# Performance work log

Hardware: AMD Instinct MI355X
Metric: run time of the kernel (lower is better)

## Reference

```python
import jax, jax.numpy as jnp
import numpy as np

EPS = 1e-8  # torch.cosine_similarity eps
TEMPERATURE = 1.0


def setup_inputs() -> dict:
    key = jax.random.key(0)
    ks = jax.random.split(key, 12)
    B = 16384
    inp = {
        "user_ids": jax.random.randint(ks[0], (B, 8), 0, 100000),
        "item_ids": jax.random.randint(ks[1], (B, 4), 0, 50000),
        "sample_weight": jax.random.uniform(ks[2], (B,), jnp.float32, 0.01, 1.0),
        "user_table": jax.random.normal(ks[3], (100000, 64), jnp.float32) * 0.05,
        "item_table": jax.random.normal(ks[4], (50000, 64), jnp.float32) * 0.05,
        "uW1": jax.random.normal(ks[5], (512, 256), jnp.float32) * 0.04,
        "ub1": jnp.zeros((256,), jnp.float32),
        "uW2": jax.random.normal(ks[6], (256, 128), jnp.float32) * 0.06,
        "ub2": jnp.zeros((128,), jnp.float32),
        "iW1": jax.random.normal(ks[7], (256, 256), jnp.float32) * 0.06,
        "ib1": jnp.zeros((256,), jnp.float32),
        "iW2": jax.random.normal(ks[8], (256, 128), jnp.float32) * 0.06,
        "ib2": jnp.zeros((128,), jnp.float32),
        "n_neg": 3,
    }
    return inp


def _tower(ids, table, W1, b1, W2, b2):
    # embedding lookup [B, F, D] -> concat -> [B, F*D], then 2-layer relu MLP
    B = ids.shape[0]
    e = table[ids].reshape(B, -1)
    h = jax.nn.relu(e @ W1 + b1)
    return jax.nn.relu(h @ W2 + b2)


def reference(user_ids, item_ids, sample_weight, user_table, item_table,
              uW1, ub1, uW2, ub2, iW1, ib1, iW2, ib2, n_neg):
    u = _tower(user_ids, user_table, uW1, ub1, uW2, ub2)  # [B, 128]
    v = _tower(item_ids, item_table, iW1, ib1, iW2, ib2)  # [B, 128]
    # cosine similarity per row (torch eps clamp on norms)
    un = jnp.maximum(jnp.linalg.norm(u, axis=1), EPS)
    vn = jnp.maximum(jnp.linalg.norm(v, axis=1), EPS)
    y = jnp.sum(u * v, axis=1) / (un * vn)
    # sampling-bias correction
    y = y - jnp.log(sample_weight)
    # vectorized wrap-around in-batch negative gather:
    # scores[i] = [y[i], y[(i+1)%B], ..., y[(i+n_neg)%B]]
    B = y.shape[0]
    idx = (jnp.arange(B)[:, None] + jnp.arange(n_neg + 1)[None, :]) % B
    scores = y[idx] / TEMPERATURE  # [B, 1+n_neg]
    return scores
```

## Files before the change

kernel.cpp:

```cpp
#include <hip/hip_runtime.h>
#include <math.h>

#define CEPS 1e-8f

typedef __attribute__((ext_vector_type(8))) short bf16x8;
typedef __attribute__((ext_vector_type(4))) float f32x4;
typedef __attribute__((ext_vector_type(4))) unsigned int u32x4;
typedef __attribute__((ext_vector_type(2))) unsigned int u32x2;

__device__ __forceinline__ unsigned short f2bf(float f) {
    unsigned u = __builtin_bit_cast(unsigned, f);
    u += 0x7fffu + ((u >> 16) & 1u);
    return (unsigned short)(u >> 16);
}

__global__ __launch_bounds__(256)
void pack_all(const float* __restrict__ uW1, const float* __restrict__ uW2,
              const float* __restrict__ iW1, const float* __restrict__ iW2,
              unsigned short* __restrict__ o1, unsigned short* __restrict__ o2,
              unsigned short* __restrict__ o3, unsigned short* __restrict__ o4)
{
    int g = blockIdx.x * 256 + threadIdx.x;
    const float* src; unsigned short* dst; int N; int base;
    if (g < 16384)      { src = uW1; dst = o1; N = 256; base = 0;     }
    else if (g < 20480) { src = uW2; dst = o2; N = 128; base = 16384; }
    else if (g < 28672) { src = iW1; dst = o3; N = 256; base = 20480; }
    else                { src = iW2; dst = o4; N = 128; base = 28672; }
    int i = g - base;
    int kg = i / N, n = i - kg * N;
    unsigned short tmp[8];
    #pragma unroll
    for (int j = 0; j < 8; ++j)
        tmp[j] = f2bf(src[(kg * 8 + j) * N + n]);
    *reinterpret_cast<bf16x8*>(dst + ((size_t)i << 3)) =
        *reinterpret_cast<bf16x8*>(tmp);
}


template<int F>
__device__ __forceinline__ void stage_emb(const int* __restrict__ ids,
                                          const float* __restrict__ table,
                                          unsigned short* e_s, int row0, int tid)
{
    constexpr int FC = F * 8;
    constexpr int IT = (32 * FC) / 512;
    int idv[IT];
    #pragma unroll
    for (int it = 0; it < IT; ++it) {
        int c = tid + it * 512;
        int r = c / FC, f = (c % FC) >> 3;
        idv[it] = ids[(row0 + r) * F + f];
    }
    #pragma unroll
    for (int it = 0; it < IT; ++it) {
        int c = tid + it * 512;
        int r = c / FC, rem = c % FC;
        const float* src = table + (size_t)idv[it] * 64 + (rem & 7) * 8;
        float4 aa = *reinterpret_cast<const float4*>(src);
        float4 bb = *reinterpret_cast<const float4*>(src + 4);
        u32x4 pk;
        pk.x = f2bf(aa.x) | ((unsigned)f2bf(aa.y) << 16);
        pk.y = f2bf(aa.z) | ((unsigned)f2bf(aa.w) << 16);
        pk.z = f2bf(bb.x) | ((unsigned)f2bf(bb.y) << 16);
        pk.w = f2bf(bb.z) | ((unsigned)f2bf(bb.w) << 16);
        int byte = r * (F * 128) + rem * 16;
        byte ^= (r & 7) << 4;
        *reinterpret_cast<u32x4*>(reinterpret_cast<char*>(e_s) + byte) = pk;
    }
}

template<int KB>
__device__ __forceinline__ bf16x8 loadA(const unsigned short* s, int ks, int ni,
                                        int l15, int l4)
{
    int row = ni * 16 + l15;
    int byte = row * (KB * 2) + ks * 64 + l4 * 16;
    byte ^= (row & 7) << 4;
    return *reinterpret_cast<const bf16x8*>(
               reinterpret_cast<const char*>(s) + byte);
}

template<int K1>
__device__ __forceinline__ void gemm1(
    const unsigned short* e_s, unsigned short* h_s,
    const unsigned short* __restrict__ W1p, const float* __restrict__ b1,
    int l15, int l4, int wl, const bf16x8 (&w01)[2][4])
{
    constexpr int NKS = K1 / 32;
    f32x4 acc[4][2];
    #pragma unroll
    for (int mi = 0; mi < 4; ++mi)
        #pragma unroll
        for (int ni = 0; ni < 2; ++ni) acc[mi][ni] = (f32x4){0.f, 0.f, 0.f, 0.f};

    const unsigned short* Wbase = W1p + ((l4 * 256 + wl * 64 + l15) << 3);
    bf16x8 wf[3][4], ef[2][2];
    #pragma unroll
    for (int mi = 0; mi < 4; ++mi) {
        wf[0][mi] = w01[0][mi];
        wf[1][mi] = w01[1][mi];
    }
    #pragma unroll
    for (int ni = 0; ni < 2; ++ni) ef[0][ni] = loadA<K1>(e_s, 0, ni, l15, l4);

    #pragma unroll
    for (int ks = 0; ks < NKS; ++ks) {
        if (ks + 2 < NKS) {
            #pragma unroll
            for (int mi = 0; mi < 4; ++mi)
                wf[(ks + 2) % 3][mi] = *reinterpret_cast<const bf16x8*>(
                    Wbase + (ks + 2) * 8192 + (mi << 7));
        }
        if (ks + 1 < NKS) {
            #pragma unroll
            for (int ni = 0; ni < 2; ++ni)
                ef[(ks + 1) & 1][ni] = loadA<K1>(e_s, ks + 1, ni, l15, l4);
        }
        __builtin_amdgcn_s_setprio(1);
        #pragma unroll
        for (int mi = 0; mi < 4; ++mi)
            #pragma unroll
            for (int ni = 0; ni < 2; ++ni)
                acc[mi][ni] = __builtin_amdgcn_mfma_f32_16x16x32_bf16(
                                  wf[ks % 3][mi], ef[ks & 1][ni], acc[mi][ni], 0, 0, 0);
        __builtin_amdgcn_s_setprio(0);
    }
    #pragma unroll
    for (int mi = 0; mi < 4; ++mi) {
        const float4 bb = *reinterpret_cast<const float4*>(
                              &b1[wl * 64 + mi * 16 + l4 * 4]);
        #pragma unroll
        for (int ni = 0; ni < 2; ++ni) {
            float v0 = acc[mi][ni][0] + bb.x; v0 = v0 > 0.f ? v0 : 0.f;
            float v1 = acc[mi][ni][1] + bb.y; v1 = v1 > 0.f ? v1 : 0.f;
            float v2 = acc[mi][ni][2] + bb.z; v2 = v2 > 0.f ? v2 : 0.f;
            float v3 = acc[mi][ni][3] + bb.w; v3 = v3 > 0.f ? v3 : 0.f;
            u32x2 d;
            d.x = f2bf(v0) | ((unsigned)f2bf(v1) << 16);
            d.y = f2bf(v2) | ((unsigned)f2bf(v3) << 16);
            int row = ni * 16 + l15;
            int w0c = wl * 64 + mi * 16 + l4 * 4;
            int byte = (row * 256 + w0c) * 2;
            byte ^= (row & 7) << 4;
            *reinterpret_cast<u32x2*>(reinterpret_cast<char*>(h_s) + byte) = d;
        }
    }
}

__device__ __forceinline__ void gemm2(
    const unsigned short* h_s, const unsigned short* __restrict__ W2p,
    f32x4 (&acc)[2][2], int l15, int l4, int wl, const bf16x8 (&w01)[2][2])
{
    #pragma unroll
    for (int mi = 0; mi < 2; ++mi)
        #pragma unroll
        for (int ni = 0; ni < 2; ++ni) acc[mi][ni] = (f32x4){0.f, 0.f, 0.f, 0.f};

    const unsigned short* Wbase = W2p + ((l4 * 128 + wl * 32 + l15) << 3);
    bf16x8 wf[3][2], hf[2][2];
    #pragma unroll
    for (int mi = 0; mi < 2; ++mi) {
        wf[0][mi] = w01[0][mi];
        wf[1][mi] = w01[1][mi];
    }
    #pragma unroll
    for (int ni = 0; ni < 2; ++ni) hf[0][ni] = loadA<256>(h_s, 0, ni, l15, l4);

    #pragma unroll
    for (int ks = 0; ks < 8; ++ks) {
        if (ks + 2 < 8) {
            #pragma unroll
            for (int mi = 0; mi < 2; ++mi)
                wf[(ks + 2) % 3][mi] = *reinterpret_cast<const bf16x8*>(
                    Wbase + (ks + 2) * 4096 + (mi << 7));
        }
        if (ks + 1 < 8) {
            #pragma unroll
            for (int ni = 0; ni < 2; ++ni)
                hf[(ks + 1) & 1][ni] = loadA<256>(h_s, ks + 1, ni, l15, l4);
        }
        __builtin_amdgcn_s_setprio(1);
        #pragma unroll
        for (int mi = 0; mi < 2; ++mi)
            #pragma unroll
            for (int ni = 0; ni < 2; ++ni)
                acc[mi][ni] = __builtin_amdgcn_mfma_f32_16x16x32_bf16(
                                  wf[ks % 3][mi], hf[ks & 1][ni], acc[mi][ni], 0, 0, 0);
        __builtin_amdgcn_s_setprio(0);
    }
}

__global__ __launch_bounds__(512, 4)
void fused_sbc(const int* __restrict__ user_ids,  const int* __restrict__ item_ids,
               const float* __restrict__ user_table, const float* __restrict__ item_table,
               const unsigned short* __restrict__ uW1p, const float* __restrict__ ub1,
               const unsigned short* __restrict__ uW2p, const float* __restrict__ ub2,
               const unsigned short* __restrict__ iW1p, const float* __restrict__ ib1,
               const unsigned short* __restrict__ iW2p, const float* __restrict__ ib2,
               const float* __restrict__ sw, float* __restrict__ out,
               int B, int nn1)
{
    __shared__ __align__(16) unsigned short smem[40960];
    unsigned short* e_u = smem;
    unsigned short* e_i = smem + 16384;
    unsigned short* h_u = smem + 24576;
    unsigned short* h_i = smem + 32768;
    float* V_lds = reinterpret_cast<float*>(smem);
    float* red   = reinterpret_cast<float*>(smem + 16384);

    const int tid  = threadIdx.x;
    const int lane = tid & 63;
    const int w    = tid >> 6;
    const int l15  = lane & 15, l4 = lane >> 4;
    const int role = w >> 2;
    const int wl   = w & 3;
    const int row0 = blockIdx.x * 32;

    const unsigned short* W1sel = role ? iW1p : uW1p;
    const unsigned short* W2sel = role ? iW2p : uW2p;

    bf16x8 w1pre[2][4];
    {
        const unsigned short* base = W1sel + ((l4 * 256 + wl * 64 + l15) << 3);
        #pragma unroll
        for (int s = 0; s < 2; ++s)
            #pragma unroll
            for (int mi = 0; mi < 4; ++mi)
                w1pre[s][mi] = *reinterpret_cast<const bf16x8*>(
                                   base + s * 8192 + (mi << 7));
    }
    stage_emb<8>(user_ids, user_table, e_u, row0, tid);
    stage_emb<4>(item_ids, item_table, e_i, row0, tid);
    __syncthreads();

    if (role == 0) gemm1<512>(e_u, h_u, uW1p, ub1, l15, l4, wl, w1pre);
    else           gemm1<256>(e_i, h_i, iW1p, ib1, l15, l4, wl, w1pre);

    bf16x8 w2pre[2][2];
    {
        const unsigned short* base = W2sel + ((l4 * 128 + wl * 32 + l15) << 3);
        #pragma unroll
        for (int s = 0; s < 2; ++s)
            #pragma unroll
            for (int mi = 0; mi < 2; ++mi)
                w2pre[s][mi] = *reinterpret_cast<const bf16x8*>(
                                   base + s * 4096 + (mi << 7));
    }
    __syncthreads();

    f32x4 acc2[2][2];
    if (role == 0) gemm2(h_u, uW2p, acc2, l15, l4, wl, w2pre);
    else           gemm2(h_i, iW2p, acc2, l15, l4, wl, w2pre);

    if (role == 1) {
        float pv[2] = {0.f, 0.f};
        #pragma unroll
        for (int mi = 0; mi < 2; ++mi) {
            const int colb = wl * 32 + mi * 16 + l4 * 4;
            const float4 bv = *reinterpret_cast<const float4*>(&ib2[colb]);
            #pragma unroll
            for (int ni = 0; ni < 2; ++ni) {
                int row = ni * 16 + l15;
                float v0 = acc2[mi][ni][0] + bv.x; v0 = v0 > 0.f ? v0 : 0.f;
                float v1 = acc2[mi][ni][1] + bv.y; v1 = v1 > 0.f ? v1 : 0.f;
                float v2 = acc2[mi][ni][2] + bv.z; v2 = v2 > 0.f ? v2 : 0.f;
                float v3 = acc2[mi][ni][3] + bv.w; v3 = v3 > 0.f ? v3 : 0.f;
                float4 vv = {v0, v1, v2, v3};
                *reinterpret_cast<float4*>(&V_lds[row * 132 + colb]) = vv;
                pv[ni] += v0 * v0 + v1 * v1 + v2 * v2 + v3 * v3;
            }
        }
        #pragma unroll
        for (int ni = 0; ni < 2; ++ni) {
            pv[ni] += __shfl_xor(pv[ni], 16);
            pv[ni] += __shfl_xor(pv[ni], 32);
        }
        if (l4 == 0) {
            #pragma unroll
            for (int ni = 0; ni < 2; ++ni)
                red[(wl * 32 + ni * 16 + l15) * 3 + 2] = pv[ni];
        }
    }
    __syncthreads();

    if (role == 0) {
        float pd[2] = {0.f, 0.f}, pu[2] = {0.f, 0.f};
        #pragma unroll
        for (int mi = 0; mi < 2; ++mi) {
            const int colb = wl * 32 + mi * 16 + l4 * 4;
            const float4 bu = *reinterpret_cast<const float4*>(&ub2[colb]);
            #pragma unroll
            for (int ni = 0; ni < 2; ++ni) {
                int row = ni * 16 + l15;
                float u0 = acc2[mi][ni][0] + bu.x; u0 = u0 > 0.f ? u0 : 0.f;
                float u1 = acc2[mi][ni][1] + bu.y; u1 = u1 > 0.f ? u1 : 0.f;
                float u2 = acc2[mi][ni][2] + bu.z; u2 = u2 > 0.f ? u2 : 0.f;
                float u3 = acc2[mi][ni][3] + bu.w; u3 = u3 > 0.f ? u3 : 0.f;
                const float4 vv = *reinterpret_cast<const float4*>(
                                      &V_lds[row * 132 + colb]);
                pd[ni] += u0 * vv.x + u1 * vv.y + u2 * vv.z + u3 * vv.w;
                pu[ni] += u0 * u0 + u1 * u1 + u2 * u2 + u3 * u3;
            }
        }
        #pragma unroll
        for (int ni = 0; ni < 2; ++ni) {
            pd[ni] += __shfl_xor(pd[ni], 16);
            pd[ni] += __shfl_xor(pd[ni], 32);
            pu[ni] += __shfl_xor(pu[ni], 16);
            pu[ni] += __shfl_xor(pu[ni], 32);
        }
        if (l4 == 0) {
            #pragma unroll
            for (int ni = 0; ni < 2; ++ni) {
                red[(wl * 32 + ni * 16 + l15) * 3 + 0] = pd[ni];
                red[(wl * 32 + ni * 16 + l15) * 3 + 1] = pu[ni];
            }
        }
    }
    __syncthreads();

    if (tid < 32) {
        int row = tid;
        float d = 0.f, su = 0.f, sv = 0.f;
        #pragma unroll
        for (int cg = 0; cg < 4; ++cg) {
            d  += red[(cg * 32 + row) * 3 + 0];
            su += red[(cg * 32 + row) * 3 + 1];
            sv += red[(cg * 32 + row) * 3 + 2];
        }
        float un = fmaxf(sqrtf(su), CEPS);
        float vn = fmaxf(sqrtf(sv), CEPS);
        int grow = row0 + row;
        float yv = d / (un * vn) - logf(sw[grow]);
        for (int j = 0; j < nn1; ++j) {
            int idx = grow - j;
            if (idx < 0) idx += B;
            out[idx * nn1 + j] = yv;
        }
    }
}

extern "C" void kernel_launch(void* const* d_in, const int* in_sizes, int n_in,
                              void* d_out, int out_size, void* d_ws, size_t ws_size,
                              hipStream_t stream)
{
    const int*   user_ids   = (const int*)  d_in[0];
    const int*   item_ids   = (const int*)  d_in[1];
    const float* sw         = (const float*)d_in[2];
    const float* user_table = (const float*)d_in[3];
    const float* item_table = (const float*)d_in[4];
    const float* uW1        = (const float*)d_in[5];
    const float* ub1        = (const float*)d_in[6];
    const float* uW2        = (const float*)d_in[7];
    const float* ub2        = (const float*)d_in[8];
    const float* iW1        = (const float*)d_in[9];
    const float* ib1        = (const float*)d_in[10];
    const float* iW2        = (const float*)d_in[11];
    const float* ib2        = (const float*)d_in[12];

    const int B   = in_sizes[2];
    const int nn1 = out_size / B;

    unsigned short* wp   = (unsigned short*)d_ws;
    unsigned short* uW1p = wp;
    unsigned short* uW2p = wp + 131072;
    unsigned short* iW1p = wp + 163840;
    unsigned short* iW2p = wp + 229376;
    float* out = (float*)d_out;

    pack_all<<<128, 256, 0, stream>>>(uW1, uW2, iW1, iW2,
                                      uW1p, uW2p, iW1p, iW2p);
    fused_sbc<<<B / 32, 512, 0, stream>>>(user_ids, item_ids,
                                          user_table, item_table,
                                          uW1p, ub1, uW2p, ub2,
                                          iW1p, ib1, iW2p, ib2,
                                          sw, out, B, nn1);
}
```

Baseline: 28.02 us.

## Feed first GEMM directly from embedding gathers, dropping the LDS staging

Removes the cooperative embedding staging into LDS and the barrier before the first GEMM. Each wave now gathers its own embedding rows from global memory straight into registers, converts them to bf16 with a cheaper rounding routine, and feeds them to the MFMAs with double-buffered prefetch. This cuts shared memory use (allowing more occupancy) and removes one sync, but every wave re-gathers the same embedding rows redundantly (four waves per role share rows), and the weight prefetch depth drops from two stages to one. The new bf16 rounding is round-half-up rather than round-to-nearest-even, which slightly changes numerics.

```diff
diff --git a/kernel.cpp b/kernel.cpp
--- a/kernel.cpp
+++ b/kernel.cpp
@@ -12,6 +12,21 @@
     unsigned u = __builtin_bit_cast(unsigned, f);
     u += 0x7fffu + ((u >> 16) & 1u);
     return (unsigned short)(u >> 16);
+}
+
+__device__ __forceinline__ unsigned pk2(float a, float b) {
+    unsigned ua = __builtin_bit_cast(unsigned, a) + 0x8000u;
+    unsigned ub = __builtin_bit_cast(unsigned, b) + 0x8000u;
+    return (ua >> 16) | (ub & 0xFFFF0000u);
+}
+
+__device__ __forceinline__ bf16x8 cvt8(const float4& lo, const float4& hi) {
+    u32x4 r;
+    r.x = pk2(lo.x, lo.y);
+    r.y = pk2(lo.z, lo.w);
+    r.z = pk2(hi.x, hi.y);
+    r.w = pk2(hi.z, hi.w);
+    return __builtin_bit_cast(bf16x8, r);
 }
 
 __global__ __launch_bounds__(256)
@@ -37,38 +52,6 @@
 }
 
 
-template<int F>
-__device__ __forceinline__ void stage_emb(const int* __restrict__ ids,
-                                          const float* __restrict__ table,
-                                          unsigned short* e_s, int row0, int tid)
-{
-    constexpr int FC = F * 8;
-    constexpr int IT = (32 * FC) / 512;
-    int idv[IT];
-    #pragma unroll
-    for (int it = 0; it < IT; ++it) {
-        int c = tid + it * 512;
-        int r = c / FC, f = (c % FC) >> 3;
-        idv[it] = ids[(row0 + r) * F + f];
-    }
-    #pragma unroll
-    for (int it = 0; it < IT; ++it) {
-        int c = tid + it * 512;
-        int r = c / FC, rem = c % FC;
-        const float* src = table + (size_t)idv[it] * 64 + (rem & 7) * 8;
-        float4 aa = *reinterpret_cast<const float4*>(src);
-        float4 bb = *reinterpret_cast<const float4*>(src + 4);
-        u32x4 pk;
-        pk.x = f2bf(aa.x) | ((unsigned)f2bf(aa.y) << 16);
-        pk.y = f2bf(aa.z) | ((unsigned)f2bf(aa.w) << 16);
-        pk.z = f2bf(bb.x) | ((unsigned)f2bf(bb.y) << 16);
-        pk.w = f2bf(bb.z) | ((unsigned)f2bf(bb.w) << 16);
-        int byte = r * (F * 128) + rem * 16;
-        byte ^= (r & 7) << 4;
-        *reinterpret_cast<u32x4*>(reinterpret_cast<char*>(e_s) + byte) = pk;
-    }
-}
-
 template<int KB>
 __device__ __forceinline__ bf16x8 loadA(const unsigned short* s, int ks, int ni,
                                         int l15, int l4)
@@ -80,49 +63,73 @@
                reinterpret_cast<const char*>(s) + byte);
 }
 
-template<int K1>
-__device__ __forceinline__ void gemm1(
-    const unsigned short* e_s, unsigned short* h_s,
+template<int F>
+__device__ __forceinline__ void gemm1_direct(
+    const int* __restrict__ ids, const float* __restrict__ table,
+    unsigned short* h_s,
     const unsigned short* __restrict__ W1p, const float* __restrict__ b1,
-    int l15, int l4, int wl, const bf16x8 (&w01)[2][4])
-{
-    constexpr int NKS = K1 / 32;
+    int row0, int l15, int l4, int wl, const bf16x8 (&w0)[4])
+{
+    constexpr int NKS = 2 * F;
     f32x4 acc[4][2];
     #pragma unroll
     for (int mi = 0; mi < 4; ++mi)
         #pragma unroll
         for (int ni = 0; ni < 2; ++ni) acc[mi][ni] = (f32x4){0.f, 0.f, 0.f, 0.f};
 
+    int idbuf[2][F];
+    #pragma unroll
+    for (int ni = 0; ni < 2; ++ni)
+        #pragma unroll
+        for (int g = 0; g < F / 4; ++g) {
+            int4 t = *reinterpret_cast<const int4*>(
+                         &ids[(row0 + ni * 16 + l15) * F + g * 4]);
+            idbuf[ni][g * 4 + 0] = t.x;
+            idbuf[ni][g * 4 + 1] = t.y;
+            idbuf[ni][g * 4 + 2] = t.z;
+            idbuf[ni][g * 4 + 3] = t.w;
+        }
+
     const unsigned short* Wbase = W1p + ((l4 * 256 + wl * 64 + l15) << 3);
-    bf16x8 wf[3][4], ef[2][2];
-    #pragma unroll
-    for (int mi = 0; mi < 4; ++mi) {
-        wf[0][mi] = w01[0][mi];
-        wf[1][mi] = w01[1][mi];
-    }
-    #pragma unroll
-    for (int ni = 0; ni < 2; ++ni) ef[0][ni] = loadA<K1>(e_s, 0, ni, l15, l4);
+    bf16x8 wf[2][4];
+    #pragma unroll
+    for (int mi = 0; mi < 4; ++mi) wf[0][mi] = w0[mi];
+
+    float4 eraw[2][2][2];
+    #pragma unroll
+    for (int ni = 0; ni < 2; ++ni) {
+        const float* p = table + (size_t)idbuf[ni][0] * 64 + l4 * 8;
+        eraw[0][ni][0] = *reinterpret_cast<const float4*>(p);
+        eraw[0][ni][1] = *reinterpret_cast<const float4*>(p + 4);
+    }
 
     #pragma unroll
     for (int ks = 0; ks < NKS; ++ks) {
-        if (ks + 2 < NKS) {
+        if (ks + 1 < NKS) {
+            #pragma unroll
+            for (int ni = 0; ni < 2; ++ni) {
+                const float* p = table
+                    + (size_t)idbuf[ni][(ks + 1) >> 1] * 64
+                    + ((ks + 1) & 1) * 32 + l4 * 8;
+                eraw[(ks + 1) & 1][ni][0] = *reinterpret_cast<const float4*>(p);
+                eraw[(ks + 1) & 1][ni][1] = *reinterpret_cast<const float4*>(p + 4);
+            }
             #pragma unroll
             for (int mi = 0; mi < 4; ++mi)
-                wf[(ks + 2) % 3][mi] = *reinterpret_cast<const bf16x8*>(
-                    Wbase + (ks + 2) * 8192 + (mi << 7));
-        }
-        if (ks + 1 < NKS) {
-            #pragma unroll
-            for (int ni = 0; ni < 2; ++ni)
-                ef[(ks + 1) & 1][ni] = loadA<K1>(e_s, ks + 1, ni, l15, l4);
-        }
+                wf[(ks + 1) & 1][mi] = *reinterpret_cast<const bf16x8*>(
+                    Wbase + (ks + 1) * 8192 + (mi << 7));
+        }
+        bf16x8 ef[2];
+        #pragma unroll
+        for (int ni = 0; ni < 2; ++ni)
+            ef[ni] = cvt8(eraw[ks & 1][ni][0], eraw[ks & 1][ni][1]);
         __builtin_amdgcn_s_setprio(1);
         #pragma unroll
         for (int mi = 0; mi < 4; ++mi)
             #pragma unroll
             for (int ni = 0; ni < 2; ++ni)
                 acc[mi][ni] = __builtin_amdgcn_mfma_f32_16x16x32_bf16(
-                                  wf[ks % 3][mi], ef[ks & 1][ni], acc[mi][ni], 0, 0, 0);
+                                  wf[ks & 1][mi], ef[ni], acc[mi][ni], 0, 0, 0);
         __builtin_amdgcn_s_setprio(0);
     }
     #pragma unroll
@@ -200,13 +207,12 @@
                const float* __restrict__ sw, float* __restrict__ out,
                int B, int nn1)
 {
-    __shared__ __align__(16) unsigned short smem[40960];
-    unsigned short* e_u = smem;
-    unsigned short* e_i = smem + 16384;
-    unsigned short* h_u = smem + 24576;
-    unsigned short* h_i = smem + 32768;
-    float* V_lds = reinterpret_cast<float*>(smem);
-    float* red   = reinterpret_cast<float*>(smem + 16384);
+    __shared__ __align__(16) unsigned short smem[25600];
+    unsigned short* h_u = smem;
+    unsigned short* h_i = smem + 8192;
+    float* V_lds = reinterpret_cast<float*>(smem + 16384);
+    float* red   = reinterpret_cast<float*>(
+                       reinterpret_cast<char*>(smem) + 49664);
 
     const int tid  = threadIdx.x;
     const int lane = tid & 63;
@@ -219,22 +225,20 @@
     const unsigned short* W1sel = role ? iW1p : uW1p;
     const unsigned short* W2sel = role ? iW2p : uW2p;
 
-    bf16x8 w1pre[2][4];
+    bf16x8 w1pre[4];
     {
         const unsigned short* base = W1sel + ((l4 * 256 + wl * 64 + l15) << 3);
         #pragma unroll
-        for (int s = 0; s < 2; ++s)
-            #pragma unroll
-            for (int mi = 0; mi < 4; ++mi)
-                w1pre[s][mi] = *reinterpret_cast<const bf16x8*>(
-                                   base + s * 8192 + (mi << 7));
-    }
-    stage_emb<8>(user_ids, user_table, e_u, row0, tid);
-    stage_emb<4>(item_ids, item_table, e_i, row0, tid);
-    __syncthreads();
-
-    if (role == 0) gemm1<512>(e_u, h_u, uW1p, ub1, l15, l4, wl, w1pre);
-    else           gemm1<256>(e_i, h_i, iW1p, ib1, l15, l4, wl, w1pre);
+        for (int mi = 0; mi < 4; ++mi)
+            w1pre[mi] = *reinterpret_cast<const bf16x8*>(base + (mi << 7));
+    }
+
+    if (role == 0)
+        gemm1_direct<8>(user_ids, user_table, h_u, uW1p, ub1,
+                        row0, l15, l4, wl, w1pre);
+    else
+        gemm1_direct<4>(item_ids, item_table, h_i, iW1p, ib1,
+                        row0, l15, l4, wl, w1pre);
 
     bf16x8 w2pre[2][2];
     {
```

After: 42.92 us. 1.53x slower.

## Double the block to 1024 threads and prefetch second tile's embeddings during GEMM

Applied to the files above, without the earlier changes.

Each block now processes 64 rows as two 32-row sub-tiles with 16 waves (8 per tower), halving each wave's output columns. Embedding gathers for the second sub-tile are issued into registers before the first sub-tile's GEMMs and written to separate LDS buffers afterwards, hiding gather latency behind MFMA work. The cost is larger LDS use (about 151 KB), which limits occupancy, plus extra register pressure from the prefetched data and an extra sync sequence. Grid size halves to B/64 blocks, which on a large-CU GPU may leave compute units idle.

```diff
diff --git a/kernel.cpp b/kernel.cpp
--- a/kernel.cpp
+++ b/kernel.cpp
@@ -37,38 +37,6 @@
 }
 
 
-template<int F>
-__device__ __forceinline__ void stage_emb(const int* __restrict__ ids,
-                                          const float* __restrict__ table,
-                                          unsigned short* e_s, int row0, int tid)
-{
-    constexpr int FC = F * 8;
-    constexpr int IT = (32 * FC) / 512;
-    int idv[IT];
-    #pragma unroll
-    for (int it = 0; it < IT; ++it) {
-        int c = tid + it * 512;
-        int r = c / FC, f = (c % FC) >> 3;
-        idv[it] = ids[(row0 + r) * F + f];
-    }
-    #pragma unroll
-    for (int it = 0; it < IT; ++it) {
-        int c = tid + it * 512;
-        int r = c / FC, rem = c % FC;
-        const float* src = table + (size_t)idv[it] * 64 + (rem & 7) * 8;
-        float4 aa = *reinterpret_cast<const float4*>(src);
-        float4 bb = *reinterpret_cast<const float4*>(src + 4);
-        u32x4 pk;
-        pk.x = f2bf(aa.x) | ((unsigned)f2bf(aa.y) << 16);
-        pk.y = f2bf(aa.z) | ((unsigned)f2bf(aa.w) << 16);
-        pk.z = f2bf(bb.x) | ((unsigned)f2bf(bb.y) << 16);
-        pk.w = f2bf(bb.z) | ((unsigned)f2bf(bb.w) << 16);
-        int byte = r * (F * 128) + rem * 16;
-        byte ^= (r & 7) << 4;
-        *reinterpret_cast<u32x4*>(reinterpret_cast<char*>(e_s) + byte) = pk;
-    }
-}
-
 template<int KB>
 __device__ __forceinline__ bf16x8 loadA(const unsigned short* s, int ks, int ni,
                                         int l15, int l4)
@@ -84,19 +52,19 @@
 __device__ __forceinline__ void gemm1(
     const unsigned short* e_s, unsigned short* h_s,
     const unsigned short* __restrict__ W1p, const float* __restrict__ b1,
-    int l15, int l4, int wl, const bf16x8 (&w01)[2][4])
+    int l15, int l4, int wl, const bf16x8 (&w01)[2][2])
 {
     constexpr int NKS = K1 / 32;
-    f32x4 acc[4][2];
-    #pragma unroll
-    for (int mi = 0; mi < 4; ++mi)
+    f32x4 acc[2][2];
+    #pragma unroll
+    for (int mi = 0; mi < 2; ++mi)
         #pragma unroll
         for (int ni = 0; ni < 2; ++ni) acc[mi][ni] = (f32x4){0.f, 0.f, 0.f, 0.f};
 
-    const unsigned short* Wbase = W1p + ((l4 * 256 + wl * 64 + l15) << 3);
-    bf16x8 wf[3][4], ef[2][2];
-    #pragma unroll
-    for (int mi = 0; mi < 4; ++mi) {
+    const unsigned short* Wbase = W1p + ((l4 * 256 + wl * 32 + l15) << 3);
+    bf16x8 wf[3][2], ef[2][2];
+    #pragma unroll
+    for (int mi = 0; mi < 2; ++mi) {
         wf[0][mi] = w01[0][mi];
         wf[1][mi] = w01[1][mi];
     }
@@ -107,7 +75,7 @@
     for (int ks = 0; ks < NKS; ++ks) {
         if (ks + 2 < NKS) {
             #pragma unroll
-            for (int mi = 0; mi < 4; ++mi)
+            for (int mi = 0; mi < 2; ++mi)
                 wf[(ks + 2) % 3][mi] = *reinterpret_cast<const bf16x8*>(
                     Wbase + (ks + 2) * 8192 + (mi << 7));
         }
@@ -118,7 +86,7 @@
         }
         __builtin_amdgcn_s_setprio(1);
         #pragma unroll
-        for (int mi = 0; mi < 4; ++mi)
+        for (int mi = 0; mi < 2; ++mi)
             #pragma unroll
             for (int ni = 0; ni < 2; ++ni)
                 acc[mi][ni] = __builtin_amdgcn_mfma_f32_16x16x32_bf16(
@@ -126,9 +94,9 @@
         __builtin_amdgcn_s_setprio(0);
     }
     #pragma unroll
-    for (int mi = 0; mi < 4; ++mi) {
+    for (int mi = 0; mi < 2; ++mi) {
         const float4 bb = *reinterpret_cast<const float4*>(
-                              &b1[wl * 64 + mi * 16 + l4 * 4]);
+                              &b1[wl * 32 + mi * 16 + l4 * 4]);
         #pragma unroll
         for (int ni = 0; ni < 2; ++ni) {
             float v0 = acc[mi][ni][0] + bb.x; v0 = v0 > 0.f ? v0 : 0.f;
@@ -139,7 +107,7 @@
             d.x = f2bf(v0) | ((unsigned)f2bf(v1) << 16);
             d.y = f2bf(v2) | ((unsigned)f2bf(v3) << 16);
             int row = ni * 16 + l15;
-            int w0c = wl * 64 + mi * 16 + l4 * 4;
+            int w0c = wl * 32 + mi * 16 + l4 * 4;
             int byte = (row * 256 + w0c) * 2;
             byte ^= (row & 7) << 4;
             *reinterpret_cast<u32x2*>(reinterpret_cast<char*>(h_s) + byte) = d;
@@ -149,31 +117,23 @@
 
 __device__ __forceinline__ void gemm2(
     const unsigned short* h_s, const unsigned short* __restrict__ W2p,
-    f32x4 (&acc)[2][2], int l15, int l4, int wl, const bf16x8 (&w01)[2][2])
-{
-    #pragma unroll
-    for (int mi = 0; mi < 2; ++mi)
-        #pragma unroll
-        for (int ni = 0; ni < 2; ++ni) acc[mi][ni] = (f32x4){0.f, 0.f, 0.f, 0.f};
-
-    const unsigned short* Wbase = W2p + ((l4 * 128 + wl * 32 + l15) << 3);
-    bf16x8 wf[3][2], hf[2][2];
-    #pragma unroll
-    for (int mi = 0; mi < 2; ++mi) {
-        wf[0][mi] = w01[0][mi];
-        wf[1][mi] = w01[1][mi];
-    }
+    f32x4 (&acc)[2], int l15, int l4, int wl, const bf16x8 (&w01)[2])
+{
+    #pragma unroll
+    for (int ni = 0; ni < 2; ++ni) acc[ni] = (f32x4){0.f, 0.f, 0.f, 0.f};
+
+    const unsigned short* Wbase = W2p + ((l4 * 128 + wl * 16 + l15) << 3);
+    bf16x8 wf[3], hf[2][2];
+    wf[0] = w01[0];
+    wf[1] = w01[1];
     #pragma unroll
     for (int ni = 0; ni < 2; ++ni) hf[0][ni] = loadA<256>(h_s, 0, ni, l15, l4);
 
     #pragma unroll
     for (int ks = 0; ks < 8; ++ks) {
-        if (ks + 2 < 8) {
-            #pragma unroll
-            for (int mi = 0; mi < 2; ++mi)
-                wf[(ks + 2) % 3][mi] = *reinterpret_cast<const bf16x8*>(
-                    Wbase + (ks + 2) * 4096 + (mi << 7));
-        }
+        if (ks + 2 < 8)
+            wf[(ks + 2) % 3] = *reinterpret_cast<const bf16x8*>(
+                                   Wbase + (ks + 2) * 4096);
         if (ks + 1 < 8) {
             #pragma unroll
             for (int ni = 0; ni < 2; ++ni)
@@ -181,16 +141,100 @@
         }
         __builtin_amdgcn_s_setprio(1);
         #pragma unroll
-        for (int mi = 0; mi < 2; ++mi)
+        for (int ni = 0; ni < 2; ++ni)
+            acc[ni] = __builtin_amdgcn_mfma_f32_16x16x32_bf16(
+                          wf[ks % 3], hf[ks & 1][ni], acc[ni], 0, 0, 0);
+        __builtin_amdgcn_s_setprio(0);
+    }
+}
+
+__device__ __forceinline__ void cosine_and_scatter(
+    const f32x4 (&acc2)[2], int role, int l15, int l4, int wl, int tid,
+    float* V_lds, float* red,
+    const float* __restrict__ ub2, const float* __restrict__ ib2,
+    const float* __restrict__ sw, float* __restrict__ out,
+    int trow0, int B, int nn1)
+{
+    const int colb = wl * 16 + l4 * 4;
+    if (role == 1) {
+        const float4 bv = *reinterpret_cast<const float4*>(&ib2[colb]);
+        float pv[2];
+        #pragma unroll
+        for (int ni = 0; ni < 2; ++ni) {
+            int row = ni * 16 + l15;
+            float v0 = acc2[ni][0] + bv.x; v0 = v0 > 0.f ? v0 : 0.f;
+            float v1 = acc2[ni][1] + bv.y; v1 = v1 > 0.f ? v1 : 0.f;
+            float v2 = acc2[ni][2] + bv.z; v2 = v2 > 0.f ? v2 : 0.f;
+            float v3 = acc2[ni][3] + bv.w; v3 = v3 > 0.f ? v3 : 0.f;
+            float4 vv = {v0, v1, v2, v3};
+            *reinterpret_cast<float4*>(&V_lds[row * 132 + colb]) = vv;
+            pv[ni] = v0 * v0 + v1 * v1 + v2 * v2 + v3 * v3;
+        }
+        #pragma unroll
+        for (int ni = 0; ni < 2; ++ni) {
+            pv[ni] += __shfl_xor(pv[ni], 16);
+            pv[ni] += __shfl_xor(pv[ni], 32);
+        }
+        if (l4 == 0) {
             #pragma unroll
             for (int ni = 0; ni < 2; ++ni)
-                acc[mi][ni] = __builtin_amdgcn_mfma_f32_16x16x32_bf16(
-                                  wf[ks % 3][mi], hf[ks & 1][ni], acc[mi][ni], 0, 0, 0);
-        __builtin_amdgcn_s_setprio(0);
-    }
-}
-
-__global__ __launch_bounds__(512, 4)
+                red[(wl * 32 + ni * 16 + l15) * 3 + 2] = pv[ni];
+        }
+    }
+    __syncthreads();
+    if (role == 0) {
+        const float4 bu = *reinterpret_cast<const float4*>(&ub2[colb]);
+        float pd[2], pu[2];
+        #pragma unroll
+        for (int ni = 0; ni < 2; ++ni) {
+            int row = ni * 16 + l15;
+            float u0 = acc2[ni][0] + bu.x; u0 = u0 > 0.f ? u0 : 0.f;
+            float u1 = acc2[ni][1] + bu.y; u1 = u1 > 0.f ? u1 : 0.f;
+            float u2 = acc2[ni][2] + bu.z; u2 = u2 > 0.f ? u2 : 0.f;
+            float u3 = acc2[ni][3] + bu.w; u3 = u3 > 0.f ? u3 : 0.f;
+            const float4 vv = *reinterpret_cast<const float4*>(
+                                  &V_lds[row * 132 + colb]);
+            pd[ni] = u0 * vv.x + u1 * vv.y + u2 * vv.z + u3 * vv.w;
+            pu[ni] = u0 * u0 + u1 * u1 + u2 * u2 + u3 * u3;
+        }
+        #pragma unroll
+        for (int ni = 0; ni < 2; ++ni) {
+            pd[ni] += __shfl_xor(pd[ni], 16);
+            pd[ni] += __shfl_xor(pd[ni], 32);
+            pu[ni] += __shfl_xor(pu[ni], 16);
+            pu[ni] += __shfl_xor(pu[ni], 32);
+        }
+        if (l4 == 0) {
+            #pragma unroll
+            for (int ni = 0; ni < 2; ++ni) {
+                red[(wl * 32 + ni * 16 + l15) * 3 + 0] = pd[ni];
+                red[(wl * 32 + ni * 16 + l15) * 3 + 1] = pu[ni];
+            }
+        }
+    }
+    __syncthreads();
+    if (tid < 32) {
+        int row = tid;
+        float d = 0.f, su = 0.f, sv = 0.f;
+        #pragma unroll
+        for (int cg = 0; cg < 8; ++cg) {
+            d  += red[(cg * 32 + row) * 3 + 0];
+            su += red[(cg * 32 + row) * 3 + 1];
+            sv += red[(cg * 32 + row) * 3 + 2];
+        }
+        float un = fmaxf(sqrtf(su), CEPS);
+        float vn = fmaxf(sqrtf(sv), CEPS);
+        int grow = trow0 + row;
+        float yv = d / (un * vn) - logf(sw[grow]);
+        for (int j = 0; j < nn1; ++j) {
+            int idx = grow - j;
+            if (idx < 0) idx += B;
+            out[idx * nn1 + j] = yv;
+        }
+    }
+}
+
+__global__ __launch_bounds__(1024, 4)
 void fused_sbc(const int* __restrict__ user_ids,  const int* __restrict__ item_ids,
                const float* __restrict__ user_table, const float* __restrict__ item_table,
                const unsigned short* __restrict__ uW1p, const float* __restrict__ ub1,
@@ -200,144 +244,153 @@
                const float* __restrict__ sw, float* __restrict__ out,
                int B, int nn1)
 {
-    __shared__ __align__(16) unsigned short smem[40960];
-    unsigned short* e_u = smem;
-    unsigned short* e_i = smem + 16384;
-    unsigned short* h_u = smem + 24576;
-    unsigned short* h_i = smem + 32768;
-    float* V_lds = reinterpret_cast<float*>(smem);
-    float* red   = reinterpret_cast<float*>(smem + 16384);
+    __shared__ __align__(16) unsigned short smem[75520];
+    unsigned short* e_u0 = smem;
+    unsigned short* e_u1 = smem + 16384;
+    unsigned short* e_i0 = smem + 32768;
+    unsigned short* e_i1 = smem + 40960;
+    unsigned short* h_u  = smem + 49152;
+    unsigned short* h_i  = smem + 57344;
+    float* V_lds = reinterpret_cast<float*>(smem + 65536);
+    float* red   = reinterpret_cast<float*>(smem + 73984);
 
     const int tid  = threadIdx.x;
     const int lane = tid & 63;
     const int w    = tid >> 6;
     const int l15  = lane & 15, l4 = lane >> 4;
-    const int role = w >> 2;
-    const int wl   = w & 3;
-    const int row0 = blockIdx.x * 32;
+    const int role = w >> 3;
+    const int wl   = w & 7;
+    const int row0 = blockIdx.x * 64;
 
     const unsigned short* W1sel = role ? iW1p : uW1p;
     const unsigned short* W2sel = role ? iW2p : uW2p;
-
-    bf16x8 w1pre[2][4];
+    const unsigned short* W1base = W1sel + ((l4 * 256 + wl * 32 + l15) << 3);
+    const unsigned short* W2base = W2sel + ((l4 * 128 + wl * 16 + l15) << 3);
+
+    bf16x8 w1pre[2][2];
+    #pragma unroll
+    for (int s = 0; s < 2; ++s)
+        #pragma unroll
+        for (int mi = 0; mi < 2; ++mi)
+            w1pre[s][mi] = *reinterpret_cast<const bf16x8*>(
+                               W1base + s * 8192 + (mi << 7));
+
     {
-        const unsigned short* base = W1sel + ((l4 * 256 + wl * 64 + l15) << 3);
-        #pragma unroll
-        for (int s = 0; s < 2; ++s)
-            #pragma unroll
-            for (int mi = 0; mi < 4; ++mi)
-                w1pre[s][mi] = *reinterpret_cast<const bf16x8*>(
-                                   base + s * 8192 + (mi << 7));
-    }
-    stage_emb<8>(user_ids, user_table, e_u, row0, tid);
-    stage_emb<4>(item_ids, item_table, e_i, row0, tid);
+        int idv[2];
+        #pragma unroll
+        for (int it = 0; it < 2; ++it) {
+            int c = tid + it * 1024;
+            idv[it] = user_ids[(row0 + (c >> 6)) * 8 + ((c & 63) >> 3)];
+        }
+        #pragma unroll
+        for (int it = 0; it < 2; ++it) {
+            int c = tid + it * 1024;
+            int r = c >> 6, rem = c & 63;
+            const float* src = user_table + (size_t)idv[it] * 64 + (rem & 7) * 8;
+            float4 aa = *reinterpret_cast<const float4*>(src);
+            float4 bb = *reinterpret_cast<const float4*>(src + 4);
+            u32x4 pk;
+            pk.x = f2bf(aa.x) | ((unsigned)f2bf(aa.y) << 16);
+            pk.y = f2bf(aa.z) | ((unsigned)f2bf(aa.w) << 16);
+            pk.z = f2bf(bb.x) | ((unsigned)f2bf(bb.y) << 16);
+            pk.w = f2bf(bb.z) | ((unsigned)f2bf(bb.w) << 16);
+            int byte = r * 1024 + rem * 16;
+            byte ^= (r & 7) << 4;
+            *reinterpret_cast<u32x4*>(reinterpret_cast<char*>(e_u0) + byte) = pk;
+        }
+        int iid = item_ids[(row0 + (tid >> 5)) * 4 + ((tid & 31) >> 3)];
+        const float* src = item_table + (size_t)iid * 64 + (tid & 7) * 8;
+        float4 aa = *reinterpret_cast<const float4*>(src);
+        float4 bb = *reinterpret_cast<const float4*>(src + 4);
+        u32x4 pk;
+        pk.x = f2bf(aa.x) | ((unsigned)f2bf(aa.y) << 16);
+        pk.y = f2bf(aa.z) | ((unsigned)f2bf(aa.w) << 16);
+        pk.z = f2bf(bb.x) | ((unsigned)f2bf(bb.y) << 16);
+        pk.w = f2bf(bb.z) | ((unsigned)f2bf(bb.w) << 16);
+        int r = tid >> 5, rem = tid & 31;
+        int byte = r * 512 + rem * 16;
+        byte ^= (r & 7) << 4;
+        *reinterpret_cast<u32x4*>(reinterpret_cast<char*>(e_i0) + byte) = pk;
+    }
     __syncthreads();
 
-    if (role == 0) gemm1<512>(e_u, h_u, uW1p, ub1, l15, l4, wl, w1pre);
-    else           gemm1<256>(e_i, h_i, iW1p, ib1, l15, l4, wl, w1pre);
-
-    bf16x8 w2pre[2][2];
+    const int trow1 = row0 + 32;
+    float4 raw[6];
     {
-        const unsigned short* base = W2sel + ((l4 * 128 + wl * 32 + l15) << 3);
-        #pragma unroll
-        for (int s = 0; s < 2; ++s)
-            #pragma unroll
-            for (int mi = 0; mi < 2; ++mi)
-                w2pre[s][mi] = *reinterpret_cast<const bf16x8*>(
-                                   base + s * 4096 + (mi << 7));
+        int c0 = tid, c1 = tid + 1024;
+        int uid0 = user_ids[(trow1 + (c0 >> 6)) * 8 + ((c0 & 63) >> 3)];
+        int uid1 = user_ids[(trow1 + (c1 >> 6)) * 8 + ((c1 & 63) >> 3)];
+        const float* p0 = user_table + (size_t)uid0 * 64 + (c0 & 7) * 8;
+        const float* p1 = user_table + (size_t)uid1 * 64 + (c1 & 7) * 8;
+        raw[0] = *reinterpret_cast<const float4*>(p0);
+        raw[1] = *reinterpret_cast<const float4*>(p0 + 4);
+        raw[2] = *reinterpret_cast<const float4*>(p1);
+        raw[3] = *reinterpret_cast<const float4*>(p1 + 4);
+        int iid = item_ids[(trow1 + (tid >> 5)) * 4 + ((tid & 31) >> 3)];
+        const float* p2 = item_table + (size_t)iid * 64 + (tid & 7) * 8;
+        raw[4] = *reinterpret_cast<const float4*>(p2);
+        raw[5] = *reinterpret_cast<const float4*>(p2 + 4);
+    }
+
+    if (role == 0) gemm1<512>(e_u0, h_u, uW1p, ub1, l15, l4, wl, w1pre);
+    else           gemm1<256>(e_i0, h_i, iW1p, ib1, l15, l4, wl, w1pre);
+
+    bf16x8 w2pre[2];
+    w2pre[0] = *reinterpret_cast<const bf16x8*>(W2base);
+    w2pre[1] = *reinterpret_cast<const bf16x8*>(W2base + 4096);
+
+    {
+        #pragma unroll
+        for (int it = 0; it < 2; ++it) {
+            int c = tid + it * 1024;
+            int r = c >> 6, rem = c & 63;
+            u32x4 pk;
+            pk.x = f2bf(raw[2 * it].x) | ((unsigned)f2bf(raw[2 * it].y) << 16);
+            pk.y = f2bf(raw[2 * it].z) | ((unsigned)f2bf(raw[2 * it].w) << 16);
+            pk.z = f2bf(raw[2 * it + 1].x) | ((unsigned)f2bf(raw[2 * it + 1].y) << 16);
+            pk.w = f2bf(raw[2 * it + 1].z) | ((unsigned)f2bf(raw[2 * it + 1].w) << 16);
+            int byte = r * 1024 + rem * 16;
+            byte ^= (r & 7) << 4;
+            *reinterpret_cast<u32x4*>(reinterpret_cast<char*>(e_u1) + byte) = pk;
+        }
+        int r = tid >> 5, rem = tid & 31;
+        u32x4 pk;
+        pk.x = f2bf(raw[4].x) | ((unsigned)f2bf(raw[4].y) << 16);
+        pk.y = f2bf(raw[4].z) | ((unsigned)f2bf(raw[4].w) << 16);
+        pk.z = f2bf(raw[5].x) | ((unsigned)f2bf(raw[5].y) << 16);
+        pk.w = f2bf(raw[5].z) | ((unsigned)f2bf(raw[5].w) << 16);
+        int byte = r * 512 + rem * 16;
+        byte ^= (r & 7) << 4;
+        *reinterpret_cast<u32x4*>(reinterpret_cast<char*>(e_i1) + byte) = pk;
     }
     __syncthreads();
 
-    f32x4 acc2[2][2];
+    f32x4 acc2[2];
     if (role == 0) gemm2(h_u, uW2p, acc2, l15, l4, wl, w2pre);
     else           gemm2(h_i, iW2p, acc2, l15, l4, wl, w2pre);
 
-    if (role == 1) {
-        float pv[2] = {0.f, 0.f};
-        #pragma unroll
-        for (int mi = 0; mi < 2; ++mi) {
-            const int colb = wl * 32 + mi * 16 + l4 * 4;
-            const float4 bv = *reinterpret_cast<const float4*>(&ib2[colb]);
-            #pragma unroll
-            for (int ni = 0; ni < 2; ++ni) {
-                int row = ni * 16 + l15;
-                float v0 = acc2[mi][ni][0] + bv.x; v0 = v0 > 0.f ? v0 : 0.f;
-                float v1 = acc2[mi][ni][1] + bv.y; v1 = v1 > 0.f ? v1 : 0.f;
-                float v2 = acc2[mi][ni][2] + bv.z; v2 = v2 > 0.f ? v2 : 0.f;
-                float v3 = acc2[mi][ni][3] + bv.w; v3 = v3 > 0.f ? v3 : 0.f;
-                float4 vv = {v0, v1, v2, v3};
-                *reinterpret_cast<float4*>(&V_lds[row * 132 + colb]) = vv;
-                pv[ni] += v0 * v0 + v1 * v1 + v2 * v2 + v3 * v3;
-            }
-        }
-        #pragma unroll
-        for (int ni = 0; ni < 2; ++ni) {
-            pv[ni] += __shfl_xor(pv[ni], 16);
-            pv[ni] += __shfl_xor(pv[ni], 32);
-        }
-        if (l4 == 0) {
-            #pragma unroll
-            for (int ni = 0; ni < 2; ++ni)
-                red[(wl * 32 + ni * 16 + l15) * 3 + 2] = pv[ni];
-        }
-    }
+    #pragma unroll
+    for (int s = 0; s < 2; ++s)
+        #pragma unroll
+        for (int mi = 0; mi < 2; ++mi)
+            w1pre[s][mi] = *reinterpret_cast<const bf16x8*>(
+                               W1base + s * 8192 + (mi << 7));
+
+    cosine_and_scatter(acc2, role, l15, l4, wl, tid, V_lds, red,
+                       ub2, ib2, sw, out, row0, B, nn1);
+
+    if (role == 0) gemm1<512>(e_u1, h_u, uW1p, ub1, l15, l4, wl, w1pre);
+    else           gemm1<256>(e_i1, h_i, iW1p, ib1, l15, l4, wl, w1pre);
+
+    w2pre[0] = *reinterpret_cast<const bf16x8*>(W2base);
+    w2pre[1] = *reinterpret_cast<const bf16x8*>(W2base + 4096);
     __syncthreads();
 
-    if (role == 0) {
-        float pd[2] = {0.f, 0.f}, pu[2] = {0.f, 0.f};
-        #pragma unroll
-        for (int mi = 0; mi < 2; ++mi) {
-            const int colb = wl * 32 + mi * 16 + l4 * 4;
-            const float4 bu = *reinterpret_cast<const float4*>(&ub2[colb]);
-            #pragma unroll
-            for (int ni = 0; ni < 2; ++ni) {
-                int row = ni * 16 + l15;
-                float u0 = acc2[mi][ni][0] + bu.x; u0 = u0 > 0.f ? u0 : 0.f;
-                float u1 = acc2[mi][ni][1] + bu.y; u1 = u1 > 0.f ? u1 : 0.f;
-                float u2 = acc2[mi][ni][2] + bu.z; u2 = u2 > 0.f ? u2 : 0.f;
-                float u3 = acc2[mi][ni][3] + bu.w; u3 = u3 > 0.f ? u3 : 0.f;
-                const float4 vv = *reinterpret_cast<const float4*>(
-                                      &V_lds[row * 132 + colb]);
-                pd[ni] += u0 * vv.x + u1 * vv.y + u2 * vv.z + u3 * vv.w;
-                pu[ni] += u0 * u0 + u1 * u1 + u2 * u2 + u3 * u3;
-            }
-        }
-        #pragma unroll
-        for (int ni = 0; ni < 2; ++ni) {
-            pd[ni] += __shfl_xor(pd[ni], 16);
-            pd[ni] += __shfl_xor(pd[ni], 32);
-            pu[ni] += __shfl_xor(pu[ni], 16);
-            pu[ni] += __shfl_xor(pu[ni], 32);
-        }
-        if (l4 == 0) {
-            #pragma unroll
-            for (int ni = 0; ni < 2; ++ni) {
-                red[(wl * 32 + ni * 16 + l15) * 3 + 0] = pd[ni];
-                red[(wl * 32 + ni * 16 + l15) * 3 + 1] = pu[ni];
-            }
-        }
-    }
-    __syncthreads();
-
-    if (tid < 32) {
-        int row = tid;
-        float d = 0.f, su = 0.f, sv = 0.f;
-        #pragma unroll
-        for (int cg = 0; cg < 4; ++cg) {
-            d  += red[(cg * 32 + row) * 3 + 0];
-            su += red[(cg * 32 + row) * 3 + 1];
-            sv += red[(cg * 32 + row) * 3 + 2];
-        }
-        float un = fmaxf(sqrtf(su), CEPS);
-        float vn = fmaxf(sqrtf(sv), CEPS);
-        int grow = row0 + row;
-        float yv = d / (un * vn) - logf(sw[grow]);
-        for (int j = 0; j < nn1; ++j) {
-            int idx = grow - j;
-            if (idx < 0) idx += B;
-            out[idx * nn1 + j] = yv;
-        }
-    }
+    if (role == 0) gemm2(h_u, uW2p, acc2, l15, l4, wl, w2pre);
+    else           gemm2(h_i, iW2p, acc2, l15, l4, wl, w2pre);
+
+    cosine_and_scatter(acc2, role, l15, l4, wl, tid, V_lds, red,
+                       ub2, ib2, sw, out, trow1, B, nn1);
 }
 
 extern "C" void kernel_launch(void* const* d_in, const int* in_sizes, int n_in,
@@ -370,9 +423,9 @@
 
     pack_all<<<128, 256, 0, stream>>>(uW1, uW2, iW1, iW2,
                                       uW1p, uW2p, iW1p, iW2p);
-    fused_sbc<<<B / 32, 512, 0, stream>>>(user_ids, item_ids,
-                                          user_table, item_table,
-                                          uW1p, ub1, uW2p, ub2,
-                                          iW1p, ib1, iW2p, ib2,
-                                          sw, out, B, nn1);
-}
+    fused_sbc<<<B / 64, 1024, 0, stream>>>(user_ids, item_ids,
+                                           user_table, item_table,
+                                           uW1p, ub1, uW2p, ub2,
+                                           iW1p, ib1, iW2p, ib2,
+                                           sw, out, B, nn1);
+}
```

New measurement: 29.95 us. 1.07x slower.
